# Kernel optimization log

Hardware: AMD Instinct MI355X
Metric: run time of the kernel (lower is better)

## Reference

```python
import jax, jax.numpy as jnp
import numpy as np

PAD = 128  # attention_limit; window = 2*PAD+1 = 257


def setup_inputs() -> dict:
    key = jax.random.key(0)
    ks = jax.random.split(key, 8)
    B, S, E = 4, 4096, 512
    x = jax.random.normal(ks[0], (B, S, E), dtype=jnp.float32)
    mask = jax.random.randint(ks[1], (B, S, 1), 0, 2, dtype=jnp.int32)
    s = 1.0 / np.sqrt(E)
    Wq = jax.random.normal(ks[2], (E, E), dtype=jnp.float32) * s
    bq = jax.random.normal(ks[3], (E,), dtype=jnp.float32) * 0.01
    Wk = jax.random.normal(ks[4], (E, E), dtype=jnp.float32) * s
    bk = jax.random.normal(ks[5], (E,), dtype=jnp.float32) * 0.01
    Wv = jax.random.normal(ks[6], (E, E), dtype=jnp.float32) * s
    bv = jax.random.normal(ks[7], (E,), dtype=jnp.float32) * 0.01
    return {"x": x, "mask": mask, "Wq": Wq, "bq": bq, "Wk": Wk, "bk": bk, "Wv": Wv, "bv": bv}


def _local_attention(x, mask, Wq, bq, Wk, bk, Wv, bv):
    B, S, E = x.shape
    pad = PAD
    blk = pad                # block size = pad so window spans exactly 3 blocks
    nb = S // blk            # S chosen as a multiple of blk
    # Padded sequence: padded key/value positions get Linear(0)=bias and are
    # UNMASKED (original pads pre_mask with value=1) -- faithfully reproduced.
    ext = jnp.pad(x, ((0, 0), (pad, pad), (0, 0)))                    # [B,S+2p,E]
    pm = jnp.pad(mask.astype(jnp.float32), ((0, 0), (pad, pad), (0, 0)),
                 constant_values=1.0)[..., 0]                          # [B,S+2p]
    q = x @ Wq + bq                                                    # [B,S,E]
    k = ext @ Wk + bk                                                  # [B,S+2p,E]
    v = ext @ Wv + bv
    qb = q.reshape(B, nb, blk, E)
    kr = k.reshape(B, nb + 2, blk, E)
    vr = v.reshape(B, nb + 2, blk, E)
    pmr = pm.reshape(B, nb + 2, blk)
    # Query block b attends key blocks b, b+1, b+2 of the padded sequence.
    kb = jnp.concatenate([kr[:, i:i + nb] for i in range(3)], axis=2)   # [B,nb,3blk,E]
    vb = jnp.concatenate([vr[:, i:i + nb] for i in range(3)], axis=2)
    pmb = jnp.concatenate([pmr[:, i:i + nb] for i in range(3)], axis=2)  # [B,nb,3blk]
    e = jnp.einsum('bnqe,bnke->bnqk', qb, kb) / jnp.sqrt(jnp.float32(E))
    e = jnp.where(pmb[:, :, None, :] == 0, jnp.float32(-1e9), e)
    # Band mask: relative position d = k_idx - blk - q_idx must satisfy |d| <= pad;
    # out-of-band gets -inf so softmax matches the exact 257-wide window.
    qi = jnp.arange(blk)[:, None]
    ki = jnp.arange(3 * blk)[None, :]
    band = jnp.abs(ki - blk - qi) <= pad                                # [blk,3blk]
    e = jnp.where(band[None, None], e, -jnp.inf)
    a = jax.nn.softmax(e, axis=-1)                                      # [B,nb,blk,3blk]
    o = jnp.einsum('bnqk,bnke->bnqe', a, vb).reshape(B, S, E)
    return jnp.where(mask == 0, jnp.float32(0.0), o)


def reference(x, mask, Wq, bq, Wk, bk, Wv, bv):
    return _local_attention(x, mask, Wq, bq, Wk, bk, Wv, bv)
```

## Files before the change

### kernel.cpp

```cpp
#include <hip/hip_runtime.h>
#include <math.h>
#include <stdint.h>

#define BATCH 4
#define SEQ   4096
#define EMB   512
#define PADW  128
#define SPAD  (SEQ + 2*PADW)
#define WIN   (3*PADW)

static constexpr float SCALE = 0.04419417382415922f;

typedef __attribute__((ext_vector_type(8))) short    s16x8;
typedef __attribute__((ext_vector_type(4))) short    s16x4;
typedef __attribute__((ext_vector_type(4))) float    f32x4;
typedef __attribute__((ext_vector_type(8))) _Float16 f16x8;

__device__ __forceinline__ unsigned short f2h(float x) {
  _Float16 h = (_Float16)x;
  return __builtin_bit_cast(unsigned short, h);
}
__device__ __forceinline__ void gload16(const void* g, void* lds) {
  __builtin_amdgcn_global_load_lds(
      (const __attribute__((address_space(1))) uint32_t*)g,
      (__attribute__((address_space(3))) uint32_t*)lds, 16, 0, 0);
}
__device__ __forceinline__ f16x8 frag64(const unsigned short* base, int row, int slot) {
  return *(const f16x8*)((const char*)base + row * 128 + ((slot ^ (row & 7)) << 4));
}

__global__ __launch_bounds__(256) void convert_x(const float* __restrict__ x,
                                                 unsigned short* __restrict__ xh) {
  size_t i = ((size_t)blockIdx.x * 256 + threadIdx.x) * 8;
  float4 a = *(const float4*)&x[i];
  float4 c = *(const float4*)&x[i + 4];
  s16x8 o;
  o[0] = (short)f2h(a.x); o[1] = (short)f2h(a.y);
  o[2] = (short)f2h(a.z); o[3] = (short)f2h(a.w);
  o[4] = (short)f2h(c.x); o[5] = (short)f2h(c.y);
  o[6] = (short)f2h(c.z); o[7] = (short)f2h(c.w);
  *(s16x8*)&xh[i] = o;
}

__global__ __launch_bounds__(256) void convert_w(const float* __restrict__ Wq,
                                                 const float* __restrict__ Wk,
                                                 const float* __restrict__ Wv,
                                                 unsigned short* __restrict__ wt) {
  const int w = blockIdx.z;
  const float* W = (w == 0) ? Wq : (w == 1) ? Wk : Wv;
  const int kt = blockIdx.x * 64, nt = blockIdx.y * 64;
  __shared__ float T[64][65];
  const int tid = threadIdx.x;
  {
    int r = tid >> 4, c4 = (tid & 15) * 4;
#pragma unroll
    for (int i = 0; i < 4; ++i) {
      float4 v = *(const float4*)&W[(size_t)(kt + r + 16 * i) * EMB + nt + c4];
      T[r + 16 * i][c4 + 0] = v.x;
      T[r + 16 * i][c4 + 1] = v.y;
      T[r + 16 * i][c4 + 2] = v.z;
      T[r + 16 * i][c4 + 3] = v.w;
    }
  }
  __syncthreads();
  {
    int n = tid >> 2, k0 = (tid & 3) * 16;
    __align__(16) unsigned short hb[16];
#pragma unroll
    for (int j = 0; j < 16; ++j) hb[j] = f2h(T[k0 + j][n]);
    size_t base = ((size_t)w * EMB + nt + n) * EMB;
    *(s16x8*)&wt[base + kt + k0]     = *(s16x8*)&hb[0];
    *(s16x8*)&wt[base + kt + k0 + 8] = *(s16x8*)&hb[8];
  }
}

__global__ __launch_bounds__(256) void proj_kernel(
    const unsigned short* __restrict__ xh,
    const unsigned short* __restrict__ wt,
    const float* __restrict__ bq, const float* __restrict__ bk, const float* __restrict__ bv,
    unsigned short* __restrict__ qh,
    unsigned short* __restrict__ kh,
    unsigned short* __restrict__ vt)
{
  int linear = blockIdx.x + 34 * (blockIdx.y + 4 * blockIdx.z);
  int swz = (linear & 7) * 204 + (linear >> 3);
  const int w  = swz % 3;
  int rest = swz / 3;
  const int mt = rest % 34;
  rest /= 34;
  const int nt = rest & 3;
  const int b  = rest >> 2;
  const float* bias = (w == 0) ? bq : (w == 1) ? bk : bv;
  const int tid = threadIdx.x, lane = tid & 63, wid = tid >> 6;
  const int t0 = mt * 128, n0 = nt * 128;

  if (mt == 0 || mt == 33) {
    if (w < 2) {
      unsigned short* om = (w == 0) ? qh : kh;
      for (int i = tid; i < 128 * 128; i += 256) {
        int r = i >> 7, n = i & 127;
        om[((size_t)b * SPAD + t0 + r) * EMB + n0 + n] = f2h(bias[n0 + n]);
      }
    } else {
      for (int i = tid; i < 128 * 128; i += 256) {
        int e = i >> 7, t = i & 127;
        vt[((size_t)b * EMB + n0 + e) * SPAD + t0 + t] = f2h(bias[n0 + e]);
      }
    }
    return;
  }

  __shared__ __align__(16) unsigned short smem[17408];
  unsigned short* At = smem;
  unsigned short* Bt = smem + 8192;

  f32x4 acc[4][4];
#pragma unroll
  for (int i = 0; i < 4; ++i)
#pragma unroll
    for (int j = 0; j < 4; ++j) acc[i][j] = (f32x4){0.f, 0.f, 0.f, 0.f};

  const int xr0 = (mt - 1) * 128;
  const int wm = wid >> 1, wn = wid & 1;

  for (int kt = 0; kt < EMB; kt += 64) {
#pragma unroll
    for (int i = 0; i < 4; ++i) {
      int c = wid * 256 + i * 64 + lane;
      int m = c >> 3, sl = (c & 7) ^ (m & 7);
      gload16(xh + ((size_t)b * SEQ + xr0 + m) * EMB + kt + sl * 8,
              (char*)At + (wid * 256 + i * 64) * 16);
    }
#pragma unroll
    for (int i = 0; i < 4; ++i) {
      int c = wid * 256 + i * 64 + lane;
      int n = c >> 3, sl = (c & 7) ^ (n & 7);
      gload16(wt + ((size_t)w * EMB + n0 + n) * EMB + kt + sl * 8,
              (char*)Bt + (wid * 256 + i * 64) * 16);
    }
    __syncthreads();
#pragma unroll
    for (int kk = 0; kk < 2; ++kk) {
      f16x8 af[4], bfr[4];
#pragma unroll
      for (int f = 0; f < 4; ++f)
        af[f] = frag64(At, wm * 64 + f * 16 + (lane & 15), kk * 4 + (lane >> 4));
#pragma unroll
      for (int f = 0; f < 4; ++f)
        bfr[f] = frag64(Bt, wn * 64 + f * 16 + (lane & 15), kk * 4 + (lane >> 4));
#pragma unroll
      for (int fm = 0; fm < 4; ++fm)
#pragma unroll
        for (int fn = 0; fn < 4; ++fn)
          acc[fm][fn] = __builtin_amdgcn_mfma_f32_16x16x32_f16(af[fm], bfr[fn], acc[fm][fn], 0, 0, 0);
    }
    __syncthreads();
  }

  if (w < 2) {
    unsigned short* om = (w == 0) ? qh : kh;
#pragma unroll
    for (int fm = 0; fm < 4; ++fm) {
      int t = t0 + wm * 64 + fm * 16 + ((lane >> 4) << 2);
#pragma unroll
      for (int fn = 0; fn < 4; ++fn) {
        int n = n0 + wn * 64 + fn * 16 + (lane & 15);
        float bsv = bias[n];
#pragma unroll
        for (int r = 0; r < 4; ++r)
          om[((size_t)b * SPAD + t + r) * EMB + n] = f2h(acc[fm][fn][r] + bsv);
      }
    }
  } else {
    unsigned short* T = smem;
#pragma unroll
    for (int fm = 0; fm < 4; ++fm) {
      int tl = wm * 64 + fm * 16 + ((lane >> 4) << 2);
#pragma unroll
      for (int fn = 0; fn < 4; ++fn) {
        int el = wn * 64 + fn * 16 + (lane & 15);
        float bsv = bias[n0 + el];
        s16x4 pk;
#pragma unroll
        for (int r = 0; r < 4; ++r) pk[r] = (short)f2h(acc[fm][fn][r] + bsv);
        *(s16x4*)&T[el * 136 + tl] = pk;
      }
    }
    __syncthreads();
#pragma unroll
    for (int it = 0; it < 8; ++it) {
      int c = it * 256 + tid;
      int e = c >> 4, t8 = (c & 15) * 8;
      s16x8 vchunk = *(s16x8*)&T[e * 136 + t8];
      *(s16x8*)&vt[((size_t)b * EMB + n0 + e) * SPAD + t0 + t8] = vchunk;
    }
  }
}

__global__ __launch_bounds__(512, 4) void attn_kernel(
    const unsigned short* __restrict__ qh,
    const unsigned short* __restrict__ kh,
    const unsigned short* __restrict__ vt,
    const int* __restrict__ mask,
    float* __restrict__ out) {
  int linear = blockIdx.x + 64 * blockIdx.y;
  linear = (linear & 7) * 32 + (linear >> 3);
  const int b  = linear >> 6;
  const int s0 = (linear & 63) * 64;
  const int nb = s0 >> 7, o = s0 & 127;
  const int t0 = nb * 128;
  const int tid = threadIdx.x, lane = tid & 63, wid = tid >> 6;

  __shared__ __align__(16) char smem[53504];
  unsigned short* P = (unsigned short*)smem;
  float* red  = (float*)(smem + 49152);
  float* red2 = (float*)(smem + 51200);
  float* invl = (float*)(smem + 53248);

  const int l15 = lane & 15;
  const int oct = (lane >> 4) << 3;
  const int kr0 = wid * 48;

  f32x4 accS[3][4];
#pragma unroll
  for (int i = 0; i < 3; ++i)
#pragma unroll
    for (int j = 0; j < 4; ++j) accS[i][j] = (f32x4){0.f, 0.f, 0.f, 0.f};

  const bool active = (kr0 < o + 320) && (kr0 + 48 > o);
  if (active) {
    const unsigned short* kp = kh + ((size_t)b * SPAD + t0 + kr0 + l15) * EMB;
    const unsigned short* qp = qh + ((size_t)b * SPAD + PADW + s0 + l15) * EMB;
#pragma unroll 4
    for (int kt = 0; kt < EMB; kt += 32) {
      f16x8 af[3], bfq[4];
#pragma unroll
      for (int f = 0; f < 3; ++f)
        af[f] = *(const f16x8*)&kp[(size_t)f * 16 * EMB + kt + oct];
#pragma unroll
      for (int f = 0; f < 4; ++f)
        bfq[f] = *(const f16x8*)&qp[(size_t)f * 16 * EMB + kt + oct];
#pragma unroll
      for (int fk = 0; fk < 3; ++fk)
#pragma unroll
        for (int fq = 0; fq < 4; ++fq)
          accS[fk][fq] = __builtin_amdgcn_mfma_f32_16x16x32_f16(af[fk], bfq[fq], accS[fk][fq], 0, 0, 0);
    }
  }

  float pmv[3][4];
#pragma unroll
  for (int fk = 0; fk < 3; ++fk) {
    int kq = kr0 + fk * 16 + ((lane >> 4) << 2);
    int tq = t0 + kq - PADW;
    int4 mv = make_int4(1, 1, 1, 1);
    if (tq >= 0 && tq < SEQ) mv = *(const int4*)&mask[(size_t)b * SEQ + tq];
    pmv[fk][0] = (float)mv.x; pmv[fk][1] = (float)mv.y;
    pmv[fk][2] = (float)mv.z; pmv[fk][3] = (float)mv.w;
  }

  float mx[4] = {-INFINITY, -INFINITY, -INFINITY, -INFINITY};
#pragma unroll
  for (int fk = 0; fk < 3; ++fk)
#pragma unroll
    for (int fq = 0; fq < 4; ++fq)
#pragma unroll
      for (int r = 0; r < 4; ++r) {
        int k = kr0 + fk * 16 + ((lane >> 4) << 2) + r;
        int p = o + fq * 16 + l15;
        float v;
        if (k < p || k > p + 2 * PADW) v = -INFINITY;
        else v = (pmv[fk][r] == 0.f) ? -1e9f : accS[fk][fq][r] * SCALE;
        accS[fk][fq][r] = v;
        mx[fq] = fmaxf(mx[fq], v);
      }
#pragma unroll
  for (int fq = 0; fq < 4; ++fq) {
    mx[fq] = fmaxf(mx[fq], __shfl_xor(mx[fq], 16));
    mx[fq] = fmaxf(mx[fq], __shfl_xor(mx[fq], 32));
  }
  if (lane < 16) {
#pragma unroll
    for (int fq = 0; fq < 4; ++fq) red[wid * 64 + fq * 16 + lane] = mx[fq];
  }
  __syncthreads();
  float M[4];
#pragma unroll
  for (int fq = 0; fq < 4; ++fq) {
    float m = -INFINITY;
#pragma unroll
    for (int ww = 0; ww < 8; ++ww) m = fmaxf(m, red[ww * 64 + fq * 16 + l15]);
    M[fq] = m;
  }
  float sm[4] = {0.f, 0.f, 0.f, 0.f};
#pragma unroll
  for (int fk = 0; fk < 3; ++fk)
#pragma unroll
    for (int fq = 0; fq < 4; ++fq)
#pragma unroll
      for (int r = 0; r < 4; ++r) {
        float pv = __expf(accS[fk][fq][r] - M[fq]);
        accS[fk][fq][r] = pv;
        sm[fq] += pv;
      }
#pragma unroll
  for (int fq = 0; fq < 4; ++fq) {
    sm[fq] += __shfl_xor(sm[fq], 16);
    sm[fq] += __shfl_xor(sm[fq], 32);
  }
  if (lane < 16) {
#pragma unroll
    for (int fq = 0; fq < 4; ++fq) red2[wid * 64 + fq * 16 + lane] = sm[fq];
  }
  __syncthreads();
  if (wid == 0 && lane < 16) {
#pragma unroll
    for (int fq = 0; fq < 4; ++fq) {
      float s = 0.f;
#pragma unroll
      for (int ww = 0; ww < 8; ++ww) s += red2[ww * 64 + fq * 16 + lane];
      invl[fq * 16 + lane] = 1.f / s;
    }
  }
#pragma unroll
  for (int fk = 0; fk < 3; ++fk)
#pragma unroll
    for (int fq = 0; fq < 4; ++fq) {
      int k0 = kr0 + fk * 16 + ((lane >> 4) << 2);
      int q = fq * 16 + l15;
      s16x4 pk;
      pk[0] = (short)f2h(accS[fk][fq][0]);
      pk[1] = (short)f2h(accS[fk][fq][1]);
      pk[2] = (short)f2h(accS[fk][fq][2]);
      pk[3] = (short)f2h(accS[fk][fq][3]);
      int sl = k0 >> 3;
      *(s16x4*)((char*)P + q * 768 + ((sl ^ (q & 7)) << 4) + ((k0 & 7) << 1)) = pk;
    }
  __syncthreads();

  f32x4 accO[4][4];
#pragma unroll
  for (int i = 0; i < 4; ++i)
#pragma unroll
    for (int j = 0; j < 4; ++j) accO[i][j] = (f32x4){0.f, 0.f, 0.f, 0.f};

  const unsigned short* vp = vt + ((size_t)b * EMB + wid * 64 + l15) * SPAD + t0;
#pragma unroll 2
  for (int kb = o; kb < o + 320; kb += 32) {
    f16x8 pa[4], vb[4];
#pragma unroll
    for (int fq = 0; fq < 4; ++fq) {
      int q = fq * 16 + l15;
      int sl = (kb >> 3) + (lane >> 4);
      pa[fq] = *(const f16x8*)((const char*)P + q * 768 + ((sl ^ (q & 7)) << 4));
    }
#pragma unroll
    for (int fe = 0; fe < 4; ++fe)
      vb[fe] = *(const f16x8*)&vp[(size_t)fe * 16 * SPAD + kb + oct];
#pragma unroll
    for (int fq = 0; fq < 4; ++fq)
#pragma unroll
      for (int fe = 0; fe < 4; ++fe)
        accO[fq][fe] = __builtin_amdgcn_mfma_f32_16x16x32_f16(pa[fq], vb[fe], accO[fq][fe], 0, 0, 0);
  }

#pragma unroll
  for (int fq = 0; fq < 4; ++fq) {
    int qq = fq * 16 + ((lane >> 4) << 2);
    int4 mq4 = *(const int4*)&mask[(size_t)b * SEQ + s0 + qq];
    int mqa[4] = {mq4.x, mq4.y, mq4.z, mq4.w};
#pragma unroll
    for (int r = 0; r < 4; ++r) {
      int q = qq + r;
      float sc = invl[q] * ((mqa[r] != 0) ? 1.f : 0.f);
#pragma unroll
      for (int fe = 0; fe < 4; ++fe) {
        int e = wid * 64 + fe * 16 + l15;
        out[((size_t)b * SEQ + s0 + q) * EMB + e] = accO[fq][fe][r] * sc;
      }
    }
  }
}

extern "C" void kernel_launch(void* const* d_in, const int* in_sizes, int n_in,
                              void* d_out, int out_size, void* d_ws, size_t ws_size,
                              hipStream_t stream) {
  const float* x  = (const float*)d_in[0];
  const int* mask = (const int*)d_in[1];
  const float* Wq = (const float*)d_in[2];
  const float* bq = (const float*)d_in[3];
  const float* Wk = (const float*)d_in[4];
  const float* bk = (const float*)d_in[5];
  const float* Wv = (const float*)d_in[6];
  const float* bv = (const float*)d_in[7];
  float* out = (float*)d_out;

  char* ws = (char*)d_ws;
  unsigned short* xh = (unsigned short*)ws;
  unsigned short* wt = (unsigned short*)(ws + 16777216);
  unsigned short* qh = (unsigned short*)(ws + 18350080);
  unsigned short* kh = (unsigned short*)(ws + 36175872);
  unsigned short* vt = (unsigned short*)(ws + 54001664);

  convert_x<<<dim3(4096), 256, 0, stream>>>(x, xh);
  convert_w<<<dim3(8, 8, 3), 256, 0, stream>>>(Wq, Wk, Wv, wt);
  proj_kernel<<<dim3(34, 4, 12), 256, 0, stream>>>(xh, wt, bq, bk, bv, qh, kh, vt);
  attn_kernel<<<dim3(SEQ / 64, BATCH), 512, 0, stream>>>(qh, kh, vt, mask, out);
}
```

Before: 180.7 us.

## Enlarge projection tiles to 256x128 and compute pad rows via zero-row loads

```diff
diff --git a/kernel.cpp b/kernel.cpp
--- a/kernel.cpp
+++ b/kernel.cpp
@@ -15,6 +15,8 @@
 typedef __attribute__((ext_vector_type(4))) short    s16x4;
 typedef __attribute__((ext_vector_type(4))) float    f32x4;
 typedef __attribute__((ext_vector_type(8))) _Float16 f16x8;
+
+__device__ __align__(16) unsigned short ZROW[8];
 
 __device__ __forceinline__ unsigned short f2h(float x) {
   _Float16 h = (_Float16)x;
@@ -74,7 +76,7 @@
   }
 }
 
-__global__ __launch_bounds__(256) void proj_kernel(
+__global__ __launch_bounds__(512) void proj_kernel(
     const unsigned short* __restrict__ xh,
     const unsigned short* __restrict__ wt,
     const float* __restrict__ bq, const float* __restrict__ bk, const float* __restrict__ bv,
@@ -82,37 +84,22 @@
     unsigned short* __restrict__ kh,
     unsigned short* __restrict__ vt)
 {
-  int linear = blockIdx.x + 34 * (blockIdx.y + 4 * blockIdx.z);
-  int swz = (linear & 7) * 204 + (linear >> 3);
-  const int w  = swz % 3;
-  int rest = swz / 3;
-  const int mt = rest % 34;
-  rest /= 34;
+  int linear = blockIdx.x + 17 * (blockIdx.y + 4 * blockIdx.z);
+  int swz = (linear & 7) * 102 + (linear >> 3);
+  const int w = swz % 3;
+  int rr = swz / 3;
+  const int mt = rr % 17;
+  int rest = rr / 17;
   const int nt = rest & 3;
   const int b  = rest >> 2;
   const float* bias = (w == 0) ? bq : (w == 1) ? bk : bv;
   const int tid = threadIdx.x, lane = tid & 63, wid = tid >> 6;
-  const int t0 = mt * 128, n0 = nt * 128;
-
-  if (mt == 0 || mt == 33) {
-    if (w < 2) {
-      unsigned short* om = (w == 0) ? qh : kh;
-      for (int i = tid; i < 128 * 128; i += 256) {
-        int r = i >> 7, n = i & 127;
-        om[((size_t)b * SPAD + t0 + r) * EMB + n0 + n] = f2h(bias[n0 + n]);
-      }
-    } else {
-      for (int i = tid; i < 128 * 128; i += 256) {
-        int e = i >> 7, t = i & 127;
-        vt[((size_t)b * EMB + n0 + e) * SPAD + t0 + t] = f2h(bias[n0 + e]);
-      }
-    }
-    return;
-  }
-
-  __shared__ __align__(16) unsigned short smem[17408];
+  const int t0 = mt * 256, n0 = nt * 128;
+  const int xr0 = t0 - PADW;
+
+  __shared__ __align__(16) unsigned short smem[24576];
   unsigned short* At = smem;
-  unsigned short* Bt = smem + 8192;
+  unsigned short* Bt = smem + 16384;
 
   f32x4 acc[4][4];
 #pragma unroll
@@ -120,23 +107,25 @@
 #pragma unroll
     for (int j = 0; j < 4; ++j) acc[i][j] = (f32x4){0.f, 0.f, 0.f, 0.f};
 
-  const int xr0 = (mt - 1) * 128;
   const int wm = wid >> 1, wn = wid & 1;
+  const int l15 = lane & 15;
 
   for (int kt = 0; kt < EMB; kt += 64) {
 #pragma unroll
     for (int i = 0; i < 4; ++i) {
-      int c = wid * 256 + i * 64 + lane;
+      int c = i * 512 + tid;
       int m = c >> 3, sl = (c & 7) ^ (m & 7);
-      gload16(xh + ((size_t)b * SEQ + xr0 + m) * EMB + kt + sl * 8,
-              (char*)At + (wid * 256 + i * 64) * 16);
-    }
-#pragma unroll
-    for (int i = 0; i < 4; ++i) {
-      int c = wid * 256 + i * 64 + lane;
+      int xr = xr0 + m;
+      const unsigned short* src = (xr >= 0 && xr < SEQ)
+          ? xh + ((size_t)b * SEQ + xr) * EMB + kt + sl * 8 : ZROW;
+      gload16(src, (char*)At + c * 16);
+    }
+#pragma unroll
+    for (int i = 0; i < 2; ++i) {
+      int c = i * 512 + tid;
       int n = c >> 3, sl = (c & 7) ^ (n & 7);
       gload16(wt + ((size_t)w * EMB + n0 + n) * EMB + kt + sl * 8,
-              (char*)Bt + (wid * 256 + i * 64) * 16);
+              (char*)Bt + c * 16);
     }
     __syncthreads();
 #pragma unroll
@@ -144,10 +133,10 @@
       f16x8 af[4], bfr[4];
 #pragma unroll
       for (int f = 0; f < 4; ++f)
-        af[f] = frag64(At, wm * 64 + f * 16 + (lane & 15), kk * 4 + (lane >> 4));
+        af[f] = frag64(At, wm * 64 + f * 16 + l15, kk * 4 + (lane >> 4));
 #pragma unroll
       for (int f = 0; f < 4; ++f)
-        bfr[f] = frag64(Bt, wn * 64 + f * 16 + (lane & 15), kk * 4 + (lane >> 4));
+        bfr[f] = frag64(Bt, wn * 64 + f * 16 + l15, kk * 4 + (lane >> 4));
 #pragma unroll
       for (int fm = 0; fm < 4; ++fm)
 #pragma unroll
@@ -164,7 +153,7 @@
       int t = t0 + wm * 64 + fm * 16 + ((lane >> 4) << 2);
 #pragma unroll
       for (int fn = 0; fn < 4; ++fn) {
-        int n = n0 + wn * 64 + fn * 16 + (lane & 15);
+        int n = n0 + wn * 64 + fn * 16 + l15;
         float bsv = bias[n];
 #pragma unroll
         for (int r = 0; r < 4; ++r)
@@ -174,25 +163,31 @@
   } else {
     unsigned short* T = smem;
 #pragma unroll
-    for (int fm = 0; fm < 4; ++fm) {
-      int tl = wm * 64 + fm * 16 + ((lane >> 4) << 2);
-#pragma unroll
-      for (int fn = 0; fn < 4; ++fn) {
-        int el = wn * 64 + fn * 16 + (lane & 15);
-        float bsv = bias[n0 + el];
-        s16x4 pk;
-#pragma unroll
-        for (int r = 0; r < 4; ++r) pk[r] = (short)f2h(acc[fm][fn][r] + bsv);
-        *(s16x4*)&T[el * 136 + tl] = pk;
-      }
-    }
-    __syncthreads();
-#pragma unroll
-    for (int it = 0; it < 8; ++it) {
-      int c = it * 256 + tid;
-      int e = c >> 4, t8 = (c & 15) * 8;
-      s16x8 vchunk = *(s16x8*)&T[e * 136 + t8];
-      *(s16x8*)&vt[((size_t)b * EMB + n0 + e) * SPAD + t0 + t8] = vchunk;
+    for (int h = 0; h < 2; ++h) {
+      if ((wm >> 1) == h) {
+#pragma unroll
+        for (int fm = 0; fm < 4; ++fm) {
+          int tl = (wm & 1) * 64 + fm * 16 + ((lane >> 4) << 2);
+#pragma unroll
+          for (int fn = 0; fn < 4; ++fn) {
+            int el = wn * 64 + fn * 16 + l15;
+            float bsv = bias[n0 + el];
+            s16x4 pk;
+#pragma unroll
+            for (int r = 0; r < 4; ++r) pk[r] = (short)f2h(acc[fm][fn][r] + bsv);
+            *(s16x4*)&T[el * 136 + tl] = pk;
+          }
+        }
+      }
+      __syncthreads();
+#pragma unroll
+      for (int it = 0; it < 4; ++it) {
+        int c = it * 512 + tid;
+        int e = c >> 4, t8 = (c & 15) * 8;
+        s16x8 vchunk = *(s16x8*)&T[e * 136 + t8];
+        *(s16x8*)&vt[((size_t)b * EMB + n0 + e) * SPAD + t0 + h * 128 + t8] = vchunk;
+      }
+      __syncthreads();
     }
   }
 }
@@ -404,6 +399,6 @@
 
   convert_x<<<dim3(4096), 256, 0, stream>>>(x, xh);
   convert_w<<<dim3(8, 8, 3), 256, 0, stream>>>(Wq, Wk, Wv, wt);
-  proj_kernel<<<dim3(34, 4, 12), 256, 0, stream>>>(xh, wt, bq, bk, bv, qh, kh, vt);
+  proj_kernel<<<dim3(17, 4, 12), 512, 0, stream>>>(xh, wt, bq, bk, bv, qh, kh, vt);
   attn_kernel<<<dim3(SEQ / 64, BATCH), 512, 0, stream>>>(qh, kh, vt, mask, out);
 }
```

Result: faster. 174.0 us (-3.7%).
